# Kernel tuning notes

Measured on AMD Instinct MI355X. Metric: run time of the kernel, lower is better.

Reference implementation:

```python
import jax, jax.numpy as jnp
import numpy as np


def _conv(x, w, b, stride, pad):
    y = jax.lax.conv_general_dilated(
        x, w, (stride, stride), [(pad, pad), (pad, pad)],
        dimension_numbers=('NCHW', 'OIHW', 'NCHW'))
    return y + b[None, :, None, None]


def _maxpool(x):
    # kernel 3, stride 2, padding 1 (torch MaxPool2d semantics)
    return jax.lax.reduce_window(
        x, -jnp.inf, jax.lax.max,
        (1, 1, 3, 3), (1, 1, 2, 2), [(0, 0), (0, 0), (1, 1), (1, 1)])


def _squash(s, eps=1e-8):
    n2 = jnp.sum(s * s, axis=-1, keepdims=True)
    return s * (n2 / (1.0 + n2)) / jnp.sqrt(n2 + eps)


def setup_inputs() -> dict:
    key = jax.random.key(0)
    ks = jax.random.split(key, 17)
    s = 0.05
    inp = {
        'x': jax.random.normal(ks[0], (128, 3, 32, 32), jnp.float32),
        'cw1': jax.random.normal(ks[1], (96, 3, 3, 3), jnp.float32) * s,
        'cb1': jnp.zeros((96,), jnp.float32),
        'cw2': jax.random.normal(ks[2], (256, 96, 3, 3), jnp.float32) * s,
        'cb2': jnp.zeros((256,), jnp.float32),
        'cw3': jax.random.normal(ks[3], (384, 256, 3, 3), jnp.float32) * s,
        'cb3': jnp.zeros((384,), jnp.float32),
        'pw': jax.random.normal(ks[4], (256, 384, 3, 3), jnp.float32) * s,  # 32 caps * 8 dim
        'pb': jnp.zeros((256,), jnp.float32),
        'Wcaps': jax.random.normal(ks[5], (100, 1152, 16, 8), jnp.float32) * s,
        'fw1': jax.random.normal(ks[6], (1600, 4096), jnp.float32) * s,
        'fb1': jnp.zeros((4096,), jnp.float32),
        'fw2': jax.random.normal(ks[7], (4096, 4096), jnp.float32) * s,
        'fb2': jnp.zeros((4096,), jnp.float32),
        'fw3': jax.random.normal(ks[8], (4096, 100), jnp.float32) * s,
        'fb3': jnp.zeros((100,), jnp.float32),
    }
    return inp


def reference(x, cw1, cb1, cw2, cb2, cw3, cb3, pw, pb, Wcaps,
              fw1, fb1, fw2, fb2, fw3, fb3):
    ROUTINGS = 3
    # AlexNet-style conv backbone
    h = jax.nn.relu(_conv(x, cw1, cb1, 1, 1))   # [B,96,32,32]
    h = _maxpool(h)                              # [B,96,16,16]
    h = jax.nn.relu(_conv(h, cw2, cb2, 1, 1))   # [B,256,16,16]
    h = _maxpool(h)                              # [B,256,8,8]
    h = jax.nn.relu(_conv(h, cw3, cb3, 1, 1))   # [B,384,8,8]
    # PrimaryCaps: conv 384 -> 32*8, k3 s1 p0 -> [B,256,6,6]
    p = _conv(h, pw, pb, 1, 0)
    u = _squash(p.reshape(p.shape[0], -1, 8))   # [B,1152,8]
    # DenseCapsule: x_hat[b,o,i,d] = sum_e W[o,i,d,e] * u[b,i,e]
    x_hat = jnp.einsum('oide,bie->boid', Wcaps, u)  # [B,100,1152,16]
    x_hat_d = jax.lax.stop_gradient(x_hat)
    b = jnp.zeros(x_hat.shape[:3], x_hat.dtype)     # [B,100,1152]
    v = None
    for r in range(ROUTINGS):
        c = jax.nn.softmax(b, axis=1)               # couple over out caps
        if r == ROUTINGS - 1:
            v = _squash(jnp.einsum('boi,boid->bod', c, x_hat))
        else:
            v = _squash(jnp.einsum('boi,boid->bod', c, x_hat_d))
            b = b + jnp.einsum('boid,bod->boi', x_hat_d, v)
    # Flatten + FC head (dropout is identity at eval)
    f = v.reshape(v.shape[0], -1)                   # [B,1600]
    f = jax.nn.relu(f @ fw1 + fb1)
    f = jax.nn.relu(f @ fw2 + fb2)
    return f @ fw3 + fb3                            # [B,100]
```

## Files before the change

### kernel.cpp

```cpp
#include <hip/hip_runtime.h>
#include <cstddef>


typedef __attribute__((ext_vector_type(8))) short bf8_t;
typedef __attribute__((ext_vector_type(4))) float f4_t;

__device__ inline void cvt_hilo8(const float* f, unsigned* h, unsigned* l)
{
  #pragma unroll
  for (int j = 0; j < 4; ++j) {
    unsigned u0 = __float_as_uint(f[2 * j]);
    unsigned u1 = __float_as_uint(f[2 * j + 1]);
    h[j] = (u0 >> 16) | (u1 & 0xFFFF0000u);
    float r0 = f[2 * j]     - __uint_as_float(u0 & 0xFFFF0000u);
    float r1 = f[2 * j + 1] - __uint_as_float(u1 & 0xFFFF0000u);
    l[j] = (__float_as_uint(r0) >> 16) | (__float_as_uint(r1) & 0xFFFF0000u);
  }
}

__device__ inline void split1(float f, unsigned short& h, unsigned short& l)
{
  unsigned u = __float_as_uint(f);
  h = (unsigned short)(u >> 16);
  float r = f - __uint_as_float(u & 0xFFFF0000u);
  l = (unsigned short)(__float_as_uint(r) >> 16);
}

__device__ inline float bf2f(unsigned short h, unsigned short l)
{
  return __uint_as_float((unsigned)h << 16) + __uint_as_float((unsigned)l << 16);
}

__device__ inline int xcd_swz(int bid, int nwg)
{
  int xcd = bid & 7, pos = bid >> 3;
  int q = nwg >> 3, r = nwg & 7;
  return (xcd < r ? xcd * (q + 1) : r * (q + 1) + (xcd - r) * q) + pos;
}

__global__ __launch_bounds__(256) void wsplit_k(
    const float* __restrict__ w, unsigned short* __restrict__ oh,
    unsigned short* __restrict__ ol, int CO, int CI)
{
  int idx = blockIdx.x * 256 + threadIdx.x;
  int ci = idx % CI;
  int t2 = idx / CI;
  int r = t2 % 9, co = t2 / 9;
  float f = w[((size_t)co * CI + ci) * 9 + r];
  unsigned short h, l;
  split1(f, h, l);
  oh[idx] = h; ol[idx] = l;
}

__global__ __launch_bounds__(256) void conv1_k(
    const float* __restrict__ x, const float* __restrict__ wt,
    const float* __restrict__ bias, unsigned short* __restrict__ oh,
    unsigned short* __restrict__ ol)
{
  int idx = blockIdx.x * 256 + threadIdx.x;
  int w = idx & 31, h = (idx >> 5) & 31, b = idx >> 10;
  int co0 = blockIdx.y * 24;

  float xv[27];
  const float* xb = x + (size_t)b * 3072;
  #pragma unroll
  for (int ci = 0; ci < 3; ++ci)
    #pragma unroll
    for (int dh = 0; dh < 3; ++dh) {
      int ih = h + dh - 1;
      #pragma unroll
      for (int dw = 0; dw < 3; ++dw) {
        int iw = w + dw - 1;
        bool ok = ((unsigned)ih < 32u) & ((unsigned)iw < 32u);
        xv[ci * 9 + dh * 3 + dw] = ok ? xb[(ci << 10) + (ih << 5) + iw] : 0.f;
      }
    }

  size_t obase = ((size_t)b * 1024 + (h << 5) + w) * 96 + co0;
  const float* wp = wt + (size_t)co0 * 27;
  #pragma unroll 2
  for (int cp = 0; cp < 12; ++cp) {
    float a0 = bias[co0 + 2 * cp], a1 = bias[co0 + 2 * cp + 1];
    #pragma unroll
    for (int k = 0; k < 27; ++k) {
      a0 += xv[k] * wp[(2 * cp) * 27 + k];
      a1 += xv[k] * wp[(2 * cp + 1) * 27 + k];
    }
    a0 = fmaxf(a0, 0.f); a1 = fmaxf(a1, 0.f);
    unsigned short h0, l0, h1, l1;
    split1(a0, h0, l0); split1(a1, h1, l1);
    *(unsigned*)(oh + obase + 2 * cp) = (unsigned)h0 | ((unsigned)h1 << 16);
    *(unsigned*)(ol + obase + 2 * cp) = (unsigned)l0 | ((unsigned)l1 << 16);
  }
}

template <int C, int H>
__global__ __launch_bounds__(256) void maxpool_bf(
    const unsigned short* __restrict__ inh, const unsigned short* __restrict__ inl,
    unsigned short* __restrict__ outh, unsigned short* __restrict__ outl)
{
  constexpr int Ho = H >> 1;
  int idx = blockIdx.x * 256 + threadIdx.x;
  int c = idx % C;
  int q = idx / C;
  int wo = q % Ho;
  int q2 = q / Ho;
  int ho = q2 % Ho, b = q2 / Ho;
  float best = -3.4e38f;
  unsigned short bh = 0, bl = 0;
  #pragma unroll
  for (int dh = 0; dh < 3; ++dh) {
    int ih = 2 * ho - 1 + dh;
    if ((unsigned)ih >= (unsigned)H) continue;
    #pragma unroll
    for (int dw = 0; dw < 3; ++dw) {
      int iw = 2 * wo - 1 + dw;
      if ((unsigned)iw >= (unsigned)H) continue;
      size_t off = ((size_t)(b * H + ih) * H + iw) * C + c;
      unsigned short uh = inh[off], ul = inl[off];
      float f = bf2f(uh, ul);
      if (f > best) { best = f; bh = uh; bl = ul; }
    }
  }
  outh[idx] = bh; outl[idx] = bl;
}

__global__ __launch_bounds__(256) void bias_split_k(
    const float* __restrict__ in, const float* __restrict__ bias,
    unsigned short* __restrict__ oh, unsigned short* __restrict__ ol,
    int C, int total2)
{
  int idx = blockIdx.x * 256 + threadIdx.x;
  if (idx >= total2) return;
  int e0 = idx * 2;
  int c = e0 % C;
  float f0 = fmaxf(in[e0] + bias[c], 0.f);
  float f1 = fmaxf(in[e0 + 1] + bias[c + 1], 0.f);
  unsigned short h0, l0, h1, l1;
  split1(f0, h0, l0); split1(f1, h1, l1);
  *(unsigned*)(oh + e0) = (unsigned)h0 | ((unsigned)h1 << 16);
  *(unsigned*)(ol + e0) = (unsigned)l0 | ((unsigned)l1 << 16);
}

template <int CI, int H, int PAD, int WO, int CO, int MT, bool SPLIT>
__global__ __launch_bounds__(256) void conv128(
    const unsigned short* __restrict__ inh, const unsigned short* __restrict__ inl,
    const unsigned short* __restrict__ wh, const unsigned short* __restrict__ wl,
    const float* __restrict__ bias, unsigned short* __restrict__ outh,
    unsigned short* __restrict__ outl, float* __restrict__ outf,
    int relu, int KC)
{
  constexpr int K = CI * 9;
  constexpr int NPIX = WO * WO;
  __shared__ uint4 Ah[512], Al[512], Bh[512], Bl[512];

  int id = xcd_swz(blockIdx.x, gridDim.x);
  int ntile = id / MT, mtile = id - ntile * MT;
  int n0 = ntile * 128, m0 = mtile * 128;
  int kbeg = SPLIT ? blockIdx.z * KC : 0;
  int kend = SPLIT ? kbeg + KC : K;

  int t = threadIdx.x;
  int lane = t & 63;
  int wave = __builtin_amdgcn_readfirstlane(t >> 6);
  int wm = wave & 1, wn = wave >> 1;
  int lr = lane & 15, lq = lane >> 4;

  int srow = (t >> 2) & 63;
  int kc8 = (t & 3) * 8;
  int sidx = srow * 4 + ((t & 3) ^ (srow & 3));

  int ih0g[2], iw0g[2];
  size_t ibaseg[2];
  #pragma unroll
  for (int g = 0; g < 2; ++g) {
    int pix = m0 + g * 64 + srow;
    int bpix = pix / NPIX, xy = pix - bpix * NPIX;
    int ho = xy / WO, wo = xy - ho * WO;
    ih0g[g] = ho - PAD; iw0g[g] = wo - PAD;
    ibaseg[g] = (size_t)bpix * H * H;
  }

  uint4 pah[2], pal_[2], pbh[2], pbl[2];
  auto loadA = [&](int k0) {
    int r = k0 / CI;
    int cib = k0 - r * CI + kc8;
    int dh = r / 3, dw = r - dh * 3;
    #pragma unroll
    for (int g = 0; g < 2; ++g) {
      int ih = ih0g[g] + dh, iw = iw0g[g] + dw;
      bool ok = ((unsigned)ih < (unsigned)H) & ((unsigned)iw < (unsigned)H);
      if (ok) {
        size_t ad = (ibaseg[g] + (size_t)ih * H + iw) * CI + cib;
        pah[g] = *(const uint4*)(inh + ad);
        pal_[g] = *(const uint4*)(inl + ad);
      } else {
        pah[g] = make_uint4(0u, 0u, 0u, 0u);
        pal_[g] = make_uint4(0u, 0u, 0u, 0u);
      }
    }
  };
  auto loadB = [&](int k0) {
    #pragma unroll
    for (int g = 0; g < 2; ++g) {
      size_t ad = (size_t)(n0 + g * 64 + srow) * K + k0 + kc8;
      pbh[g] = *(const uint4*)(wh + ad);
      pbl[g] = *(const uint4*)(wl + ad);
    }
  };

  loadA(kbeg); loadB(kbeg);
  f4_t acc[4][4];
  #pragma unroll
  for (int mt = 0; mt < 4; ++mt)
    #pragma unroll
    for (int nt = 0; nt < 4; ++nt) acc[mt][nt] = (f4_t)0.0f;

  for (int k0 = kbeg; k0 < kend; k0 += 32) {
    if (k0 > kbeg) __syncthreads();
    Ah[sidx] = pah[0]; Ah[256 + sidx] = pah[1];
    Al[sidx] = pal_[0]; Al[256 + sidx] = pal_[1];
    Bh[sidx] = pbh[0]; Bh[256 + sidx] = pbh[1];
    Bl[sidx] = pbl[0]; Bl[256 + sidx] = pbl[1];
    __syncthreads();
    if (k0 + 32 < kend) { loadA(k0 + 32); loadB(k0 + 32); }

    int xk = lq ^ (lr & 3);
    int aBase = wm * 256 + lr * 4 + xk;
    int bBase = wn * 256 + lr * 4 + xk;
    bf8_t bvh[4], bvl[4];
    #pragma unroll
    for (int nt = 0; nt < 4; ++nt) {
      bvh[nt] = *(const bf8_t*)&Bh[bBase + nt * 64];
      bvl[nt] = *(const bf8_t*)&Bl[bBase + nt * 64];
    }
    #pragma unroll
    for (int mt = 0; mt < 4; ++mt) {
      bf8_t avh = *(const bf8_t*)&Ah[aBase + mt * 64];
      bf8_t avl = *(const bf8_t*)&Al[aBase + mt * 64];
      #pragma unroll
      for (int nt = 0; nt < 4; ++nt) {
        acc[mt][nt] = __builtin_amdgcn_mfma_f32_16x16x32_bf16(avh, bvh[nt], acc[mt][nt], 0, 0, 0);
        acc[mt][nt] = __builtin_amdgcn_mfma_f32_16x16x32_bf16(avh, bvl[nt], acc[mt][nt], 0, 0, 0);
        acc[mt][nt] = __builtin_amdgcn_mfma_f32_16x16x32_bf16(avl, bvh[nt], acc[mt][nt], 0, 0, 0);
      }
    }
  }

  #pragma unroll
  for (int mt = 0; mt < 4; ++mt)
    #pragma unroll
    for (int nt = 0; nt < 4; ++nt) {
      #pragma unroll
      for (int r = 0; r < 4; ++r) {
        int m = m0 + wm * 64 + mt * 16 + lq * 4 + r;
        int n = n0 + wn * 64 + nt * 16 + lr;
        size_t oidx = (size_t)m * CO + n;
        if (SPLIT) {
          atomicAdd(outf + oidx, acc[mt][nt][r]);
        } else {
          float vv = acc[mt][nt][r] + bias[n];
          if (relu) vv = fmaxf(vv, 0.f);
          unsigned short h, l;
          split1(vv, h, l);
          outh[oidx] = h; outl[oidx] = l;
        }
      }
    }
}

__global__ __launch_bounds__(256) void fc_mfma(
    const float* __restrict__ A, const float* __restrict__ W,
    float* __restrict__ C, int K, int N, int KC)
{
  __shared__ uint4 Ah[256], Al[256], Bh[256], Bl[256];
  int n0 = blockIdx.x * 64, m0 = blockIdx.y * 64;
  int kbeg = blockIdx.z * KC, kend = kbeg + KC;
  int t = threadIdx.x;
  int lane = t & 63;
  int wave = __builtin_amdgcn_readfirstlane(t >> 6);
  int wm = wave & 1, wn = wave >> 1;
  int lr = lane & 15, lq = lane >> 4;
  int smA = t >> 2, sgA = t & 3;

  float fa[8], fb[8];
  auto loadA = [&](int k0) {
    const float4* ap = (const float4*)(A + (size_t)(m0 + smA) * K + k0 + sgA * 8);
    float4 a0 = ap[0], a1 = ap[1];
    fa[0] = a0.x; fa[1] = a0.y; fa[2] = a0.z; fa[3] = a0.w;
    fa[4] = a1.x; fa[5] = a1.y; fa[6] = a1.z; fa[7] = a1.w;
  };
  auto loadB = [&](int k0) {
    const float* wp = W + (size_t)(k0 + wave * 8) * N + n0 + lane;
    #pragma unroll
    for (int j = 0; j < 8; ++j) fb[j] = wp[(size_t)j * N];
  };

  loadA(kbeg); loadB(kbeg);
  f4_t acc[2][2];
  #pragma unroll
  for (int mt = 0; mt < 2; ++mt)
    #pragma unroll
    for (int nt = 0; nt < 2; ++nt) acc[mt][nt] = (f4_t)0.0f;

  for (int k0 = kbeg; k0 < kend; k0 += 32) {
    if (k0 > kbeg) __syncthreads();
    unsigned ha[4], la[4], hb[4], lb[4];
    cvt_hilo8(fa, ha, la);
    cvt_hilo8(fb, hb, lb);
    Ah[sgA * 64 + smA] = make_uint4(ha[0], ha[1], ha[2], ha[3]);
    Al[sgA * 64 + smA] = make_uint4(la[0], la[1], la[2], la[3]);
    Bh[wave * 64 + lane] = make_uint4(hb[0], hb[1], hb[2], hb[3]);
    Bl[wave * 64 + lane] = make_uint4(lb[0], lb[1], lb[2], lb[3]);
    __syncthreads();
    if (k0 + 32 < kend) { loadA(k0 + 32); loadB(k0 + 32); }
    bf8_t av_h[2], av_l[2], bv_h[2], bv_l[2];
    #pragma unroll
    for (int mt = 0; mt < 2; ++mt) {
      int ui = lq * 64 + wm * 32 + mt * 16 + lr;
      av_h[mt] = *(const bf8_t*)&Ah[ui];
      av_l[mt] = *(const bf8_t*)&Al[ui];
    }
    #pragma unroll
    for (int nt = 0; nt < 2; ++nt) {
      int ui = lq * 64 + wn * 32 + nt * 16 + lr;
      bv_h[nt] = *(const bf8_t*)&Bh[ui];
      bv_l[nt] = *(const bf8_t*)&Bl[ui];
    }
    #pragma unroll
    for (int mt = 0; mt < 2; ++mt)
      #pragma unroll
      for (int nt = 0; nt < 2; ++nt) {
        acc[mt][nt] = __builtin_amdgcn_mfma_f32_16x16x32_bf16(av_h[mt], bv_h[nt], acc[mt][nt], 0, 0, 0);
        acc[mt][nt] = __builtin_amdgcn_mfma_f32_16x16x32_bf16(av_h[mt], bv_l[nt], acc[mt][nt], 0, 0, 0);
        acc[mt][nt] = __builtin_amdgcn_mfma_f32_16x16x32_bf16(av_l[mt], bv_h[nt], acc[mt][nt], 0, 0, 0);
      }
  }
  #pragma unroll
  for (int mt = 0; mt < 2; ++mt)
    #pragma unroll
    for (int nt = 0; nt < 2; ++nt) {
      #pragma unroll
      for (int r = 0; r < 4; ++r) {
        int m = m0 + wm * 32 + mt * 16 + lq * 4 + r;
        int n = n0 + wn * 32 + nt * 16 + lr;
        atomicAdd(C + (size_t)m * N + n, acc[mt][nt][r]);
      }
    }
}

__global__ __launch_bounds__(256) void squash8_k(
    const float* __restrict__ p, const float* __restrict__ pb,
    float* __restrict__ ut)
{
  int idx = blockIdx.x * 256 + threadIdx.x;
  if (idx >= 147456) return;
  int b = idx & 127, i = idx >> 7;
  float pv[8];
  #pragma unroll
  for (int e = 0; e < 8; ++e) {
    int f = i * 8 + e;
    int co = f / 36, pix = f - co * 36;
    pv[e] = p[((size_t)b * 36 + pix) * 256 + co] + pb[co];
  }
  float n2 = 0.f;
  #pragma unroll
  for (int e = 0; e < 8; ++e) n2 += pv[e] * pv[e];
  float sc = (n2 / (1.f + n2)) * rsqrtf(n2 + 1e-8f);
  #pragma unroll
  for (int e = 0; e < 8; ++e)
    ut[(size_t)i * 1024 + e * 128 + b] = pv[e] * sc;
}

__global__ __launch_bounds__(256) void caps_squash16(
    const float* __restrict__ s, float* __restrict__ v, float* __restrict__ vt)
{
  int idx = blockIdx.x * 256 + threadIdx.x;
  if (idx >= 12800) return;
  int b = idx / 100, o = idx % 100;
  const float4* sp = (const float4*)(s + (size_t)idx * 16);
  float4 a = sp[0], bb = sp[1], c = sp[2], d = sp[3];
  float n2 = a.x * a.x + a.y * a.y + a.z * a.z + a.w * a.w +
             bb.x * bb.x + bb.y * bb.y + bb.z * bb.z + bb.w * bb.w +
             c.x * c.x + c.y * c.y + c.z * c.z + c.w * c.w +
             d.x * d.x + d.y * d.y + d.z * d.z + d.w * d.w;
  float sc = (n2 / (1.f + n2)) * rsqrtf(n2 + 1e-8f);
  float vv[16] = {a.x, a.y, a.z, a.w, bb.x, bb.y, bb.z, bb.w,
                  c.x, c.y, c.z, c.w, d.x, d.y, d.z, d.w};
  float4* vp = (float4*)(v + (size_t)idx * 16);
  float4 o0 = {vv[0] * sc, vv[1] * sc, vv[2] * sc, vv[3] * sc};
  float4 o1 = {vv[4] * sc, vv[5] * sc, vv[6] * sc, vv[7] * sc};
  float4 o2 = {vv[8] * sc, vv[9] * sc, vv[10] * sc, vv[11] * sc};
  float4 o3 = {vv[12] * sc, vv[13] * sc, vv[14] * sc, vv[15] * sc};
  vp[0] = o0; vp[1] = o1; vp[2] = o2; vp[3] = o3;
  #pragma unroll
  for (int dd = 0; dd < 16; ++dd)
    vt[((size_t)o * 16 + dd) * 128 + b] = vv[dd] * sc;
}

__global__ __launch_bounds__(256) void caps_spass_mfma(
    const float* __restrict__ W, const float* __restrict__ ut,
    const float* __restrict__ ct, float* __restrict__ s, int uniform)
{
  __shared__ uint4 Ah[512], Al[512];
  int o = blockIdx.x, ks = blockIdx.y;
  int t = threadIdx.x;
  int lane = t & 63;
  int wave = __builtin_amdgcn_readfirstlane(t >> 6);
  int lr = lane & 15, lq = lane >> 4;
  int b = t & 127, half = t >> 7;
  int i0 = ks * 144;

  float fu[16], fc[2], fw[8];
  auto loadUC = [&](int j) {
    int ib = i0 + j * 4 + half * 2;
    #pragma unroll
    for (int q = 0; q < 2; ++q) {
      int i = ib + q;
      #pragma unroll
      for (int e = 0; e < 8; ++e)
        fu[q * 8 + e] = ut[(size_t)i * 1024 + e * 128 + b];
      fc[q] = uniform ? 0.01f : ct[((size_t)o * 1152 + i) * 128 + b];
    }
  };
  auto loadW = [&](int j) {
    int i = i0 + j * 4 + lq;
    const float4* wp = (const float4*)(W + (((size_t)o * 1152 + i) * 16 + lr) * 8);
    float4 w0 = wp[0], w1 = wp[1];
    fw[0] = w0.x; fw[1] = w0.y; fw[2] = w0.z; fw[3] = w0.w;
    fw[4] = w1.x; fw[5] = w1.y; fw[6] = w1.z; fw[7] = w1.w;
  };

  loadUC(0); loadW(0);
  f4_t acc[2];
  acc[0] = (f4_t)0.0f; acc[1] = (f4_t)0.0f;

  for (int j = 0; j < 36; ++j) {
    float cu[16];
    #pragma unroll
    for (int q = 0; q < 2; ++q)
      #pragma unroll
      for (int e = 0; e < 8; ++e)
        cu[q * 8 + e] = fc[q] * fu[q * 8 + e];
    unsigned h0[4], l0[4], h1[4], l1[4], wh[4], wl[4];
    cvt_hilo8(cu, h0, l0);
    cvt_hilo8(cu + 8, h1, l1);
    cvt_hilo8(fw, wh, wl);
    uint4 uwh = make_uint4(wh[0], wh[1], wh[2], wh[3]);
    uint4 uwl = make_uint4(wl[0], wl[1], wl[2], wl[3]);
    bf8_t bfh = *(const bf8_t*)&uwh;
    bf8_t bfl = *(const bf8_t*)&uwl;
    if (j > 0) __syncthreads();
    Ah[(half * 2 + 0) * 128 + b] = make_uint4(h0[0], h0[1], h0[2], h0[3]);
    Al[(half * 2 + 0) * 128 + b] = make_uint4(l0[0], l0[1], l0[2], l0[3]);
    Ah[(half * 2 + 1) * 128 + b] = make_uint4(h1[0], h1[1], h1[2], h1[3]);
    Al[(half * 2 + 1) * 128 + b] = make_uint4(l1[0], l1[1], l1[2], l1[3]);
    __syncthreads();
    if (j + 1 < 36) { loadUC(j + 1); loadW(j + 1); }
    #pragma unroll
    for (int mt = 0; mt < 2; ++mt) {
      int bidx = wave * 16 + mt * 64 + lr;
      bf8_t avh = *(const bf8_t*)&Ah[lq * 128 + bidx];
      bf8_t avl = *(const bf8_t*)&Al[lq * 128 + bidx];
      acc[mt] = __builtin_amdgcn_mfma_f32_16x16x32_bf16(avh, bfh, acc[mt], 0, 0, 0);
      acc[mt] = __builtin_amdgcn_mfma_f32_16x16x32_bf16(avh, bfl, acc[mt], 0, 0, 0);
      acc[mt] = __builtin_amdgcn_mfma_f32_16x16x32_bf16(avl, bfh, acc[mt], 0, 0, 0);
    }
  }
  #pragma unroll
  for (int mt = 0; mt < 2; ++mt)
    #pragma unroll
    for (int r = 0; r < 4; ++r) {
      int bb = wave * 16 + mt * 64 + lq * 4 + r;
      atomicAdd(s + ((size_t)bb * 100 + o) * 16 + lr, acc[mt][r]);
    }
}

__global__ __launch_bounds__(256) void caps_bupdate(
    const float* __restrict__ W, const float* __restrict__ ut,
    const float* __restrict__ vt, float* __restrict__ blogt, int accum)
{
  __shared__ __align__(16) float Wt[64 * 160];
  int o = blockIdx.x, ic = blockIdx.y;
  int t = threadIdx.x;
  int lane = t & 63;
  int wave = __builtin_amdgcn_readfirstlane(t >> 6);
  int lr = lane & 15, lq = lane >> 4;
  int dhalf = (lq & 1) << 3;
  int hl = lq >> 1;

  {
    const float4* Wg = (const float4*)(W + ((size_t)o * 1152 + (size_t)ic * 64) * 128);
    for (int l = t; l < 2048; l += 256) {
      float4 w = Wg[l];
      int li = l >> 5;
      int rem = l & 31;
      int d = rem >> 1;
      int e0 = (rem & 1) << 2;
      float* dst = &Wt[li * 160 + e0 * 20 + d];
      dst[0] = w.x; dst[20] = w.y; dst[40] = w.z; dst[60] = w.w;
    }
  }

  bf8_t B1[8], B2[8];
  #pragma unroll
  for (int nt = 0; nt < 8; ++nt) {
    int b = nt * 16 + lr;
    float vv[8];
    #pragma unroll
    for (int j = 0; j < 8; ++j)
      vv[j] = vt[((size_t)o * 16 + dhalf + j) * 128 + b];
    unsigned h[4], l2[4];
    cvt_hilo8(vv, h, l2);
    uint4 uh = make_uint4(h[0], h[1], h[2], h[3]);
    uint4 ul = (lq < 2) ? make_uint4(l2[0], l2[1], l2[2], l2[3])
                        : make_uint4(0u, 0u, 0u, 0u);
    B1[nt] = *(const bf8_t*)&uh;
    B2[nt] = *(const bf8_t*)&ul;
  }
  __syncthreads();

  unsigned lomask = hl ? 0xFFFF0000u : 0u;

  for (int mi = 0; mi < 8; ++mi) {
    int mt = wave * 8 + mi;
    int liA = mt * 2 + (lr >> 3);
    int eA = lr & 7;
    const float* wp = &Wt[liA * 160 + eA * 20 + dhalf];
    float4 wa = *(const float4*)wp;
    float4 wb = *(const float4*)(wp + 4);
    float fw[8] = {wa.x, wa.y, wa.z, wa.w, wb.x, wb.y, wb.z, wb.w};
    unsigned ha[4];
    #pragma unroll
    for (int j = 0; j < 4; ++j) {
      float f0 = fw[2 * j], f1 = fw[2 * j + 1];
      f0 -= __uint_as_float(__float_as_uint(f0) & lomask);
      f1 -= __uint_as_float(__float_as_uint(f1) & lomask);
      ha[j] = (__float_as_uint(f0) >> 16) | (__float_as_uint(f1) & 0xFFFF0000u);
    }
    uint4 ua = make_uint4(ha[0], ha[1], ha[2], ha[3]);
    bf8_t A = *(const bf8_t*)&ua;

    int gi = ic * 64 + mt * 2 + hl;
    const float* up = ut + (size_t)gi * 1024 + (size_t)(((lq & 1) << 2)) * 128;
    #pragma unroll
    for (int nt = 0; nt < 8; ++nt) {
      f4_t acc = (f4_t)0.0f;
      acc = __builtin_amdgcn_mfma_f32_16x16x32_bf16(A, B1[nt], acc, 0, 0, 0);
      acc = __builtin_amdgcn_mfma_f32_16x16x32_bf16(A, B2[nt], acc, 0, 0, 0);
      int b = nt * 16 + lr;
      float p = acc[0] * up[b] + acc[1] * up[128 + b] +
                acc[2] * up[256 + b] + acc[3] * up[384 + b];
      p += __shfl_xor(p, 16);
      if (!(lq & 1)) {
        size_t off = ((size_t)o * 1152 + gi) * 128 + b;
        if (accum) blogt[off] += p; else blogt[off] = p;
      }
    }
  }
}

__global__ __launch_bounds__(256) void caps_softmax(
    const float* __restrict__ blogt, float* __restrict__ ct)
{
  int idx = blockIdx.x * 256 + threadIdx.x;
  if (idx >= 147456) return;
  const float* bp = blogt + idx;
  float m = -3.4e38f;
  for (int o = 0; o < 100; ++o) m = fmaxf(m, bp[(size_t)o * 147456]);
  float sum = 0.f;
  for (int o = 0; o < 100; ++o) sum += __expf(bp[(size_t)o * 147456] - m);
  float inv = 1.f / sum;
  for (int o = 0; o < 100; ++o)
    ct[(size_t)o * 147456 + idx] = __expf(bp[(size_t)o * 147456] - m) * inv;
}

__global__ __launch_bounds__(256) void bias_act_k(
    float* __restrict__ C, const float* __restrict__ bias, int N, int total, int relu)
{
  int idx = blockIdx.x * 256 + threadIdx.x;
  if (idx >= total) return;
  float vv = C[idx] + bias[idx % N];
  if (relu) vv = fmaxf(vv, 0.f);
  C[idx] = vv;
}

__global__ __launch_bounds__(128) void fc3_seed(
    const float* __restrict__ bias, float* __restrict__ out)
{
  int idx = blockIdx.x * 128 + threadIdx.x;
  if (idx < 12800) out[idx] = bias[idx % 100];
}

__global__ __launch_bounds__(128) void fc3_sk(
    const float* __restrict__ A, const float* __restrict__ W,
    float* __restrict__ out)
{
  __shared__ float Al[1024];
  int m = blockIdx.x, z = blockIdx.y, t = threadIdx.x;
  int kbeg = z * 1024;
  const float* ap = A + (size_t)m * 4096 + kbeg;
  for (int l = t; l < 1024; l += 128) Al[l] = ap[l];
  __syncthreads();
  if (t < 100) {
    float acc = 0.f;
    const float* wp = W + (size_t)kbeg * 100 + t;
    #pragma unroll 8
    for (int k = 0; k < 1024; ++k) acc += Al[k] * wp[(size_t)k * 100];
    atomicAdd(out + m * 100 + t, acc);
  }
}

extern "C" void kernel_launch(void* const* d_in, const int* in_sizes, int n_in,
                              void* d_out, int out_size, void* d_ws, size_t ws_size,
                              hipStream_t stream)
{
  (void)in_sizes; (void)n_in; (void)out_size; (void)ws_size;
  const float* x   = (const float*)d_in[0];
  const float* cw1 = (const float*)d_in[1];
  const float* cb1 = (const float*)d_in[2];
  const float* cw2 = (const float*)d_in[3];
  const float* cb2 = (const float*)d_in[4];
  const float* cw3 = (const float*)d_in[5];
  const float* cb3 = (const float*)d_in[6];
  const float* pw  = (const float*)d_in[7];
  const float* pb  = (const float*)d_in[8];
  const float* Wc  = (const float*)d_in[9];
  const float* fw1 = (const float*)d_in[10];
  const float* fb1 = (const float*)d_in[11];
  const float* fw2 = (const float*)d_in[12];
  const float* fb2 = (const float*)d_in[13];
  const float* fw3 = (const float*)d_in[14];
  const float* fb3 = (const float*)d_in[15];
  float* ws = (float*)d_ws;

  const size_t OFF_A  = 0;
  const size_t OFF_B  = 12582912;
  const size_t OFF_U  = 15728640;
  const size_t OFF_P  = 16908288;
  const size_t OFF_C  = 18087936;
  const size_t OFF_V  = 32833536;
  const size_t OFF_S  = 33038336;
  const size_t OFF_F1 = 33243136;
  const size_t OFF_F2 = 33767424;

  float* ut    = ws + OFF_U;
  float* p     = ws + OFF_P;
  float* vt    = ws + OFF_P;
  float* ct    = ws + OFF_C;
  float* v     = ws + OFF_V;
  float* s     = ws + OFF_S;
  float* f1    = ws + OFF_F1;
  float* f2    = ws + OFF_F2;
  float* blogt = ws + OFF_A;

  unsigned short* h1h  = (unsigned short*)(ws + OFF_A);
  unsigned short* h1l  = h1h + 12582912;
  unsigned short* mp1h = (unsigned short*)(ws + OFF_B);
  unsigned short* mp1l = mp1h + 3145728;
  unsigned short* h2h  = (unsigned short*)(ws + OFF_A);
  unsigned short* h2l  = h2h + 8388608;
  unsigned short* mp2h = (unsigned short*)(ws + OFF_B);
  unsigned short* mp2l = mp2h + 2097152;
  unsigned short* h3h  = (unsigned short*)(ws + OFF_A);
  unsigned short* h3l  = h3h + 3145728;

  unsigned short* wc2h = (unsigned short*)(ws + OFF_C);
  unsigned short* wc2l = wc2h + 221184;
  unsigned short* wc3h = wc2l + 221184;
  unsigned short* wc3l = wc3h + 884736;
  unsigned short* pwth = wc3l + 884736;
  unsigned short* pwtl = pwth + 884736;
  float* h3f = ws + OFF_C + 2097152;

  hipMemsetAsync(p,   0, (size_t)1179648 * 4, stream);
  hipMemsetAsync(h3f, 0, (size_t)3145728 * 4, stream);
  hipMemsetAsync(f1,  0, (size_t)524288 * 4, stream);
  hipMemsetAsync(f2,  0, (size_t)524288 * 4, stream);

  wsplit_k<<<864, 256, 0, stream>>>(cw2, wc2h, wc2l, 256, 96);
  wsplit_k<<<3456, 256, 0, stream>>>(cw3, wc3h, wc3l, 384, 256);
  wsplit_k<<<3456, 256, 0, stream>>>(pw,  pwth, pwtl, 256, 384);

  conv1_k<<<dim3(512, 4), 256, 0, stream>>>(x, cw1, cb1, h1h, h1l);
  maxpool_bf<96, 32><<<12288, 256, 0, stream>>>(h1h, h1l, mp1h, mp1l);
  conv128<96, 16, 1, 16, 256, 256, false><<<512, 256, 0, stream>>>(
      mp1h, mp1l, wc2h, wc2l, cb2, h2h, h2l, nullptr, 1, 0);
  maxpool_bf<256, 16><<<8192, 256, 0, stream>>>(h2h, h2l, mp2h, mp2l);
  conv128<256, 8, 1, 8, 384, 64, true><<<dim3(192, 1, 4), 256, 0, stream>>>(
      mp2h, mp2l, wc3h, wc3l, cb3, nullptr, nullptr, h3f, 0, 576);
  bias_split_k<<<6144, 256, 0, stream>>>(h3f, cb3, h3h, h3l, 384, 1572864);
  conv128<384, 8, 0, 6, 256, 36, true><<<dim3(72, 1, 6), 256, 0, stream>>>(
      h3h, h3l, pwth, pwtl, pb, nullptr, nullptr, p, 0, 576);
  squash8_k<<<576, 256, 0, stream>>>(p, pb, ut);

  for (int r = 0; r < 3; ++r) {
    hipMemsetAsync(s, 0, (size_t)204800 * 4, stream);
    if (r == 0) {
      caps_spass_mfma<<<dim3(100, 8), 256, 0, stream>>>(Wc, ut, ut , s, 1);
    } else {
      caps_softmax<<<576, 256, 0, stream>>>(blogt, ct);
      caps_spass_mfma<<<dim3(100, 8), 256, 0, stream>>>(Wc, ut, ct, s, 0);
    }
    caps_squash16<<<50, 256, 0, stream>>>(s, v, vt);
    if (r < 2)
      caps_bupdate<<<dim3(100, 18), 256, 0, stream>>>(Wc, ut, vt, blogt, r);
  }

  fc_mfma<<<dim3(64, 2, 2), 256, 0, stream>>>(v,  fw1, f1, 1600, 4096, 800);
  bias_act_k<<<2048, 256, 0, stream>>>(f1, fb1, 4096, 524288, 1);
  fc_mfma<<<dim3(64, 2, 4), 256, 0, stream>>>(f1, fw2, f2, 4096, 4096, 1024);
  bias_act_k<<<2048, 256, 0, stream>>>(f2, fb2, 4096, 524288, 1);
  fc3_seed<<<100, 128, 0, stream>>>(fb3, (float*)d_out);
  fc3_sk<<<dim3(128, 4), 128, 0, stream>>>(f2, fw3, (float*)d_out);
}
```

Before: 1.095 ms.

## Replace split-K atomics with per-slice scratch planes reduced in consumer kernels

Split-K partial sums in the convs, FC layers and the capsule s-pass are now written with plain stores to separate scratch planes instead of atomicAdd, and the consumer kernels (bias_split, squash8, caps_squash16, new bias_reduce) sum the planes. This removes the memset launches and atomic contention, and makes the reductions deterministic. In exchange the consumers read several times more data. The conv3 split also changes from 4 to 3 slices (KC 768).

New measurement: 1.155 ms. 1.05x slower.

```diff
diff --git a/kernel.cpp b/kernel.cpp
--- a/kernel.cpp
+++ b/kernel.cpp
@@ -128,18 +128,36 @@
 __global__ __launch_bounds__(256) void bias_split_k(
     const float* __restrict__ in, const float* __restrict__ bias,
     unsigned short* __restrict__ oh, unsigned short* __restrict__ ol,
-    int C, int total2)
+    int C, int total2, int nz, size_t plane)
 {
   int idx = blockIdx.x * 256 + threadIdx.x;
   if (idx >= total2) return;
   int e0 = idx * 2;
   int c = e0 % C;
-  float f0 = fmaxf(in[e0] + bias[c], 0.f);
-  float f1 = fmaxf(in[e0 + 1] + bias[c + 1], 0.f);
+  float f0 = 0.f, f1 = 0.f;
+  for (int z = 0; z < nz; ++z) {
+    f0 += in[z * plane + e0];
+    f1 += in[z * plane + e0 + 1];
+  }
+  f0 = fmaxf(f0 + bias[c], 0.f);
+  f1 = fmaxf(f1 + bias[c + 1], 0.f);
   unsigned short h0, l0, h1, l1;
   split1(f0, h0, l0); split1(f1, h1, l1);
   *(unsigned*)(oh + e0) = (unsigned)h0 | ((unsigned)h1 << 16);
   *(unsigned*)(ol + e0) = (unsigned)l0 | ((unsigned)l1 << 16);
+}
+
+__global__ __launch_bounds__(256) void bias_reduce_k(
+    const float* __restrict__ in, const float* __restrict__ bias,
+    float* __restrict__ out, int N, int total, int relu, int nz, size_t plane)
+{
+  int idx = blockIdx.x * 256 + threadIdx.x;
+  if (idx >= total) return;
+  float vv = 0.f;
+  for (int z = 0; z < nz; ++z) vv += in[z * plane + idx];
+  vv += bias[idx % N];
+  if (relu) vv = fmaxf(vv, 0.f);
+  out[idx] = vv;
 }
 
 template <int CI, int H, int PAD, int WO, int CO, int MT, bool SPLIT>
@@ -148,7 +166,7 @@
     const unsigned short* __restrict__ wh, const unsigned short* __restrict__ wl,
     const float* __restrict__ bias, unsigned short* __restrict__ outh,
     unsigned short* __restrict__ outl, float* __restrict__ outf,
-    int relu, int KC)
+    int relu, int KC, size_t plane)
 {
   constexpr int K = CI * 9;
   constexpr int NPIX = WO * WO;
@@ -159,6 +177,7 @@
   int n0 = ntile * 128, m0 = mtile * 128;
   int kbeg = SPLIT ? blockIdx.z * KC : 0;
   int kend = SPLIT ? kbeg + KC : K;
+  float* outz = SPLIT ? outf + (size_t)blockIdx.z * plane : outf;
 
   int t = threadIdx.x;
   int lane = t & 63;
@@ -257,7 +276,7 @@
         int n = n0 + wn * 64 + nt * 16 + lr;
         size_t oidx = (size_t)m * CO + n;
         if (SPLIT) {
-          atomicAdd(outf + oidx, acc[mt][nt][r]);
+          outz[oidx] = acc[mt][nt][r];
         } else {
           float vv = acc[mt][nt][r] + bias[n];
           if (relu) vv = fmaxf(vv, 0.f);
@@ -271,11 +290,12 @@
 
 __global__ __launch_bounds__(256) void fc_mfma(
     const float* __restrict__ A, const float* __restrict__ W,
-    float* __restrict__ C, int K, int N, int KC)
+    float* __restrict__ C, int K, int N, int KC, size_t plane)
 {
   __shared__ uint4 Ah[256], Al[256], Bh[256], Bl[256];
   int n0 = blockIdx.x * 64, m0 = blockIdx.y * 64;
   int kbeg = blockIdx.z * KC, kend = kbeg + KC;
+  float* Cz = C + (size_t)blockIdx.z * plane;
   int t = threadIdx.x;
   int lane = t & 63;
   int wave = __builtin_amdgcn_readfirstlane(t >> 6);
@@ -344,7 +364,7 @@
       for (int r = 0; r < 4; ++r) {
         int m = m0 + wm * 32 + mt * 16 + lq * 4 + r;
         int n = n0 + wn * 32 + nt * 16 + lr;
-        atomicAdd(C + (size_t)m * N + n, acc[mt][nt][r]);
+        Cz[(size_t)m * N + n] = acc[mt][nt][r];
       }
     }
 }
@@ -361,7 +381,11 @@
   for (int e = 0; e < 8; ++e) {
     int f = i * 8 + e;
     int co = f / 36, pix = f - co * 36;
-    pv[e] = p[((size_t)b * 36 + pix) * 256 + co] + pb[co];
+    size_t base = ((size_t)b * 36 + pix) * 256 + co;
+    float s = 0.f;
+    #pragma unroll
+    for (int z = 0; z < 6; ++z) s += p[(size_t)z * 1179648 + base];
+    pv[e] = s + pb[co];
   }
   float n2 = 0.f;
   #pragma unroll
@@ -378,15 +402,22 @@
   int idx = blockIdx.x * 256 + threadIdx.x;
   if (idx >= 12800) return;
   int b = idx / 100, o = idx % 100;
-  const float4* sp = (const float4*)(s + (size_t)idx * 16);
-  float4 a = sp[0], bb = sp[1], c = sp[2], d = sp[3];
-  float n2 = a.x * a.x + a.y * a.y + a.z * a.z + a.w * a.w +
-             bb.x * bb.x + bb.y * bb.y + bb.z * bb.z + bb.w * bb.w +
-             c.x * c.x + c.y * c.y + c.z * c.z + c.w * c.w +
-             d.x * d.x + d.y * d.y + d.z * d.z + d.w * d.w;
+  float vv[16];
+  #pragma unroll
+  for (int d = 0; d < 16; ++d) vv[d] = 0.f;
+  #pragma unroll
+  for (int z = 0; z < 8; ++z) {
+    const float4* sp = (const float4*)(s + (size_t)z * 204800 + (size_t)idx * 16);
+    float4 a = sp[0], bb = sp[1], c = sp[2], d4 = sp[3];
+    vv[0] += a.x;  vv[1] += a.y;  vv[2] += a.z;  vv[3] += a.w;
+    vv[4] += bb.x; vv[5] += bb.y; vv[6] += bb.z; vv[7] += bb.w;
+    vv[8] += c.x;  vv[9] += c.y;  vv[10] += c.z; vv[11] += c.w;
+    vv[12] += d4.x; vv[13] += d4.y; vv[14] += d4.z; vv[15] += d4.w;
+  }
+  float n2 = 0.f;
+  #pragma unroll
+  for (int d = 0; d < 16; ++d) n2 += vv[d] * vv[d];
   float sc = (n2 / (1.f + n2)) * rsqrtf(n2 + 1e-8f);
-  float vv[16] = {a.x, a.y, a.z, a.w, bb.x, bb.y, bb.z, bb.w,
-                  c.x, c.y, c.z, c.w, d.x, d.y, d.z, d.w};
   float4* vp = (float4*)(v + (size_t)idx * 16);
   float4 o0 = {vv[0] * sc, vv[1] * sc, vv[2] * sc, vv[3] * sc};
   float4 o1 = {vv[4] * sc, vv[5] * sc, vv[6] * sc, vv[7] * sc};
@@ -410,6 +441,7 @@
   int lr = lane & 15, lq = lane >> 4;
   int b = t & 127, half = t >> 7;
   int i0 = ks * 144;
+  float* sz = s + (size_t)ks * 204800;
 
   float fu[16], fc[2], fw[8];
   auto loadUC = [&](int j) {
@@ -472,7 +504,7 @@
     #pragma unroll
     for (int r = 0; r < 4; ++r) {
       int bb = wave * 16 + mt * 64 + lq * 4 + r;
-      atomicAdd(s + ((size_t)bb * 100 + o) * 16 + lr, acc[mt][r]);
+      sz[((size_t)bb * 100 + o) * 16 + lr] = acc[mt][r];
     }
 }
 
@@ -573,16 +605,6 @@
   float inv = 1.f / sum;
   for (int o = 0; o < 100; ++o)
     ct[(size_t)o * 147456 + idx] = __expf(bp[(size_t)o * 147456] - m) * inv;
-}
-
-__global__ __launch_bounds__(256) void bias_act_k(
-    float* __restrict__ C, const float* __restrict__ bias, int N, int total, int relu)
-{
-  int idx = blockIdx.x * 256 + threadIdx.x;
-  if (idx >= total) return;
-  float vv = C[idx] + bias[idx % N];
-  if (relu) vv = fmaxf(vv, 0.f);
-  C[idx] = vv;
 }
 
 __global__ __launch_bounds__(128) void fc3_seed(
@@ -645,14 +667,15 @@
   const size_t OFF_F2 = 33767424;
 
   float* ut    = ws + OFF_U;
-  float* p     = ws + OFF_P;
   float* vt    = ws + OFF_P;
   float* ct    = ws + OFF_C;
   float* v     = ws + OFF_V;
-  float* s     = ws + OFF_S;
+  float* sz    = ws + OFF_B;
   float* f1    = ws + OFF_F1;
   float* f2    = ws + OFF_F2;
   float* blogt = ws + OFF_A;
+  float* fcz   = ws + OFF_C;
+  (void)OFF_S;
 
   unsigned short* h1h  = (unsigned short*)(ws + OFF_A);
   unsigned short* h1l  = h1h + 12582912;
@@ -671,12 +694,7 @@
   unsigned short* wc3l = wc3h + 884736;
   unsigned short* pwth = wc3l + 884736;
   unsigned short* pwtl = pwth + 884736;
-  float* h3f = ws + OFF_C + 2097152;
-
-  hipMemsetAsync(p,   0, (size_t)1179648 * 4, stream);
-  hipMemsetAsync(h3f, 0, (size_t)3145728 * 4, stream);
-  hipMemsetAsync(f1,  0, (size_t)524288 * 4, stream);
-  hipMemsetAsync(f2,  0, (size_t)524288 * 4, stream);
+  float* zscr = ws + OFF_C + 2097152;
 
   wsplit_k<<<864, 256, 0, stream>>>(cw2, wc2h, wc2l, 256, 96);
   wsplit_k<<<3456, 256, 0, stream>>>(cw3, wc3h, wc3l, 384, 256);
@@ -685,32 +703,31 @@
   conv1_k<<<dim3(512, 4), 256, 0, stream>>>(x, cw1, cb1, h1h, h1l);
   maxpool_bf<96, 32><<<12288, 256, 0, stream>>>(h1h, h1l, mp1h, mp1l);
   conv128<96, 16, 1, 16, 256, 256, false><<<512, 256, 0, stream>>>(
-      mp1h, mp1l, wc2h, wc2l, cb2, h2h, h2l, nullptr, 1, 0);
+      mp1h, mp1l, wc2h, wc2l, cb2, h2h, h2l, nullptr, 1, 0, 0);
   maxpool_bf<256, 16><<<8192, 256, 0, stream>>>(h2h, h2l, mp2h, mp2l);
-  conv128<256, 8, 1, 8, 384, 64, true><<<dim3(192, 1, 4), 256, 0, stream>>>(
-      mp2h, mp2l, wc3h, wc3l, cb3, nullptr, nullptr, h3f, 0, 576);
-  bias_split_k<<<6144, 256, 0, stream>>>(h3f, cb3, h3h, h3l, 384, 1572864);
+  conv128<256, 8, 1, 8, 384, 64, true><<<dim3(192, 1, 3), 256, 0, stream>>>(
+      mp2h, mp2l, wc3h, wc3l, cb3, nullptr, nullptr, zscr, 0, 768, 3145728);
+  bias_split_k<<<6144, 256, 0, stream>>>(zscr, cb3, h3h, h3l, 384, 1572864, 3, 3145728);
   conv128<384, 8, 0, 6, 256, 36, true><<<dim3(72, 1, 6), 256, 0, stream>>>(
-      h3h, h3l, pwth, pwtl, pb, nullptr, nullptr, p, 0, 576);
-  squash8_k<<<576, 256, 0, stream>>>(p, pb, ut);
+      h3h, h3l, pwth, pwtl, pb, nullptr, nullptr, zscr, 0, 576, 1179648);
+  squash8_k<<<576, 256, 0, stream>>>(zscr, pb, ut);
 
   for (int r = 0; r < 3; ++r) {
-    hipMemsetAsync(s, 0, (size_t)204800 * 4, stream);
     if (r == 0) {
-      caps_spass_mfma<<<dim3(100, 8), 256, 0, stream>>>(Wc, ut, ut , s, 1);
+      caps_spass_mfma<<<dim3(100, 8), 256, 0, stream>>>(Wc, ut, ut , sz, 1);
     } else {
       caps_softmax<<<576, 256, 0, stream>>>(blogt, ct);
-      caps_spass_mfma<<<dim3(100, 8), 256, 0, stream>>>(Wc, ut, ct, s, 0);
-    }
-    caps_squash16<<<50, 256, 0, stream>>>(s, v, vt);
+      caps_spass_mfma<<<dim3(100, 8), 256, 0, stream>>>(Wc, ut, ct, sz, 0);
+    }
+    caps_squash16<<<50, 256, 0, stream>>>(sz, v, vt);
     if (r < 2)
       caps_bupdate<<<dim3(100, 18), 256, 0, stream>>>(Wc, ut, vt, blogt, r);
   }
 
-  fc_mfma<<<dim3(64, 2, 2), 256, 0, stream>>>(v,  fw1, f1, 1600, 4096, 800);
-  bias_act_k<<<2048, 256, 0, stream>>>(f1, fb1, 4096, 524288, 1);
-  fc_mfma<<<dim3(64, 2, 4), 256, 0, stream>>>(f1, fw2, f2, 4096, 4096, 1024);
-  bias_act_k<<<2048, 256, 0, stream>>>(f2, fb2, 4096, 524288, 1);
+  fc_mfma<<<dim3(64, 2, 2), 256, 0, stream>>>(v,  fw1, fcz, 1600, 4096, 800, 524288);
+  bias_reduce_k<<<2048, 256, 0, stream>>>(fcz, fb1, f1, 4096, 524288, 1, 2, 524288);
+  fc_mfma<<<dim3(64, 2, 4), 256, 0, stream>>>(f1, fw2, fcz, 4096, 4096, 1024, 524288);
+  bias_reduce_k<<<2048, 256, 0, stream>>>(fcz, fb2, f2, 4096, 524288, 1, 4, 524288);
   fc3_seed<<<100, 128, 0, stream>>>(fb3, (float*)d_out);
   fc3_sk<<<dim3(128, 4), 128, 0, stream>>>(f2, fw3, (float*)d_out);
 }
```
